# Kernel tuning notes

Measured on AMD Instinct MI355X. Metric: run time of the kernel, lower is better.

Reference implementation:

```python
import jax, jax.numpy as jnp
import numpy as np

B, T, E, H, QKV = 4, 2048, 1024, 16, 64
D = E // H  # head_dim = 64


def setup_inputs() -> dict:
    key = jax.random.key(0)
    k1, k2, k3, k4 = jax.random.split(key, 4)
    scale = 1.0 / np.sqrt(D)
    x = jax.random.normal(k1, (B, T, E), dtype=jnp.float32)
    W_q = jax.random.normal(k2, (QKV, D), dtype=jnp.float32) * scale
    W_k = jax.random.normal(k3, (QKV, D), dtype=jnp.float32) * scale
    W_v = jax.random.normal(k4, (QKV, D), dtype=jnp.float32) * scale
    return {"x": x, "W_q": W_q, "W_k": W_k, "W_v": W_v}


def reference(x, W_q, W_k, W_v):
    Bx, Tx, Ex = x.shape
    d = Ex // H
    # [B,T,E] -> [B,H,T,D]  (same as torch view + permute(0,2,1,3))
    xh = x.reshape(Bx, Tx, H, d).transpose(0, 2, 1, 3)
    # Shared per-head projections: Linear(d -> qkv_dim), weight stored [out,in]
    Q = jnp.einsum("bhtd,qd->bhtq", xh, W_q)
    K = jnp.einsum("bhtd,qd->bhtq", xh, W_k)
    V = jnp.einsum("bhtd,qd->bhtq", xh, W_v)
    # NOTE: original scales by head_dim**0.5, not qkv_dim**0.5
    scores = jnp.einsum("bhtq,bhsq->bhts", Q, K) / jnp.asarray(d, x.dtype) ** 0.5
    attn = jax.nn.softmax(scores, axis=-1)
    out = jnp.einsum("bhts,bhsq->bhtq", attn, V) + V  # attention + V residual
    # per-head concat on last dim == head-major merge: [B,H,T,Q] -> [B,T,H*Q]
    return out.transpose(0, 2, 1, 3).reshape(Bx, Tx, H * W_q.shape[0])
```

## Files before the change

### kernel.cpp

```cpp
#include <hip/hip_runtime.h>

#define T_SEQ 2048
#define N_B   4
#define N_H   16
#define D_H   64
#define EMB   1024
#define CSC   0.18033688011f

typedef __attribute__((ext_vector_type(8))) short   vshort8;
typedef __attribute__((ext_vector_type(4))) float   vfloat4;
typedef __attribute__((ext_vector_type(16))) float  vfloat16;

__device__ __forceinline__ ushort f2bf(float f) {
  union { float f; unsigned u; } v; v.f = f;
  unsigned u = v.u;
  return (ushort)((u + 0x7fffu + ((u >> 16) & 1u)) >> 16);
}
__device__ __forceinline__ unsigned pk2bf(float a, float b) {
  return (unsigned)f2bf(a) | ((unsigned)f2bf(b) << 16);
}
__device__ __forceinline__ float bf2f(ushort b) {
  union { unsigned u; float f; } v; v.u = ((unsigned)b) << 16;
  return v.f;
}
__device__ __forceinline__ float fexp2(float x) {
#if __has_builtin(__builtin_amdgcn_exp2f)
  return __builtin_amdgcn_exp2f(x);
#else
  return exp2f(x);
#endif
}
__device__ __forceinline__ unsigned permhi(float hi, float lo) {
  union { float f; unsigned u; } a, b; a.f = hi; b.f = lo;
#if __has_builtin(__builtin_amdgcn_perm)
  return __builtin_amdgcn_perm(a.u, b.u, 0x07060302u);
#else
  return (a.u & 0xFFFF0000u) | (b.u >> 16);
#endif
}
__device__ __forceinline__ void plswap(unsigned &a, unsigned &b) {
  asm("v_permlane32_swap_b32 %0, %1" : "+v"(a), "+v"(b));
}
__device__ __forceinline__ vshort8 cvt8(const float* p) {
  float4 w0 = *(const float4*)(p);
  float4 w1 = *(const float4*)(p + 4);
  vshort8 t;
  t[0] = (short)f2bf(w0.x); t[1] = (short)f2bf(w0.y);
  t[2] = (short)f2bf(w0.z); t[3] = (short)f2bf(w0.w);
  t[4] = (short)f2bf(w1.x); t[5] = (short)f2bf(w1.y);
  t[6] = (short)f2bf(w1.z); t[7] = (short)f2bf(w1.w);
  return t;
}


__global__ void wconv(const float* __restrict__ Wq, const float* __restrict__ Wk,
                      const float* __restrict__ Wv, ushort* __restrict__ Wb) {
  const int lane = threadIdx.x & 63;
  const int l15  = lane & 15;
  const int quad = lane >> 4;
  const float* Ws[3] = {Wq, Wk, Wv};
#pragma unroll
  for (int m = 0; m < 3; ++m)
#pragma unroll
    for (int kc = 0; kc < 2; ++kc)
#pragma unroll
      for (int nt = 0; nt < 4; ++nt) {
        vshort8 t = cvt8(Ws[m] + (nt * 16 + l15) * D_H + kc * 32 + quad * 8);
        *(vshort8*)(&Wb[(((m * 2 + kc) * 4 + nt) * 64 + lane) * 8]) = t;
      }
}

__global__ __launch_bounds__(256, 4) void proj_qkv(
    const float* __restrict__ x, const ushort* __restrict__ Wb,
    uint2* __restrict__ Qb, uint2* __restrict__ Kb, uint2* __restrict__ Vb) {
  const int wid  = threadIdx.x >> 6;
  const int lane = threadIdx.x & 63;
  const int l15  = lane & 15;
  const int q    = lane >> 4;
  const int gw    = blockIdx.x * 4 + wid;
  const int strip = gw >> 4;
  const int hd    = gw & 15;
  const int r0    = strip * 16;
  const int b     = r0 >> 11;
  const int bh    = b * N_H + hd;
  const int ts    = (r0 & (T_SEQ - 1)) >> 4;

  vshort8 afr[2];
  {
    const float* xp = x + (size_t)(r0 + l15) * EMB + hd * D_H + q * 8;
    afr[0] = cvt8(xp);
    afr[1] = cvt8(xp + 32);
  }

  uint2* Bs[3] = {Qb, Kb, Vb};
#pragma unroll
  for (int m = 0; m < 3; ++m) {
    vshort8 wf[2][4];
#pragma unroll
    for (int kc = 0; kc < 2; ++kc)
#pragma unroll
      for (int nt = 0; nt < 4; ++nt)
        wf[kc][nt] = *(const vshort8*)(&Wb[(((m * 2 + kc) * 4 + nt) * 64 + lane) * 8]);
    vfloat4 acc[4];
#pragma unroll
    for (int nt = 0; nt < 4; ++nt) acc[nt] = (vfloat4){0.f, 0.f, 0.f, 0.f};
#pragma unroll
    for (int kc = 0; kc < 2; ++kc)
#pragma unroll
      for (int nt = 0; nt < 4; ++nt)
        acc[nt] = (m < 2)
          ? __builtin_amdgcn_mfma_f32_16x16x32_bf16(wf[kc][nt], afr[kc], acc[nt], 0, 0, 0)
          : __builtin_amdgcn_mfma_f32_16x16x32_bf16(afr[kc], wf[kc][nt], acc[nt], 0, 0, 0);
    uint2* B = Bs[m];
#pragma unroll
    for (int nt = 0; nt < 4; ++nt) {
      vfloat4 a = acc[nt];
      if (m == 0) { a[0] *= CSC; a[1] *= CSC; a[2] *= CSC; a[3] *= CSC; }
      uint2 w;
      w.x = pk2bf(a[0], a[1]);
      w.y = pk2bf(a[2], a[3]);
      size_t idx;
      if (m < 2) {
        idx = ((size_t)(bh * 64 + (ts >> 1)) * 4 + nt) * 128
              + (l15 + 16 * (ts & 1)) * 4 + q;
      } else {
        idx = (((size_t)(bh * 32 + (ts >> 2)) * 4 + (ts & 3)) * 2 + (nt >> 1)) * 128
              + 64 * (nt & 1) + l15 * 4 + q;
      }
      B[idx] = w;
    }
  }
}

__device__ __forceinline__ void load_k(vshort8 (&kf)[2][4], const uint4* __restrict__ Kb,
                                       int bh, int ss, int lo) {
#pragma unroll
  for (int sb = 0; sb < 2; ++sb)
#pragma unroll
    for (int ds = 0; ds < 4; ++ds)
      kf[sb][ds] = *(const vshort8*)&Kb[((size_t)(bh * 64 + 2 * ss + sb) * 4 + ds) * 64 + lo];
}
__device__ __forceinline__ void load_v(vshort8 (&vf)[4][2], const uint4* __restrict__ Vb,
                                       int bh, int ss, int lo) {
#pragma unroll
  for (int st = 0; st < 4; ++st)
#pragma unroll
    for (int db = 0; db < 2; ++db)
      vf[st][db] = *(const vshort8*)&Vb[(((size_t)(bh * 32 + ss) * 4 + st) * 2 + db) * 64 + lo];
}

__device__ __forceinline__ void tile_compute(
    const vshort8 (&kf)[2][4], const vshort8 (&vf)[4][2], const vshort8 (&qf)[2][4],
    vfloat16 (&oacc)[2][2], float (&lsum)[2], int h) {
#pragma unroll
  for (int tb = 0; tb < 2; ++tb) {
    vfloat16 sacc[2];
#pragma unroll
    for (int sb = 0; sb < 2; ++sb)
#pragma unroll
      for (int i = 0; i < 16; ++i) sacc[sb][i] = 0.f;
#pragma unroll
    for (int sb = 0; sb < 2; ++sb)
#pragma unroll
      for (int ds = 0; ds < 4; ++ds)
        sacc[sb] = __builtin_amdgcn_mfma_f32_32x32x16_bf16(kf[sb][ds], qf[tb][ds], sacc[sb], 0, 0, 0);

    float p[2][16];
    float s0 = 0.f, s1 = 0.f, s2 = 0.f, s3 = 0.f;
#pragma unroll
    for (int sb = 0; sb < 2; ++sb)
#pragma unroll
      for (int r = 0; r < 16; r += 4) {
        p[sb][r + 0] = fexp2(sacc[sb][r + 0]); s0 += p[sb][r + 0];
        p[sb][r + 1] = fexp2(sacc[sb][r + 1]); s1 += p[sb][r + 1];
        p[sb][r + 2] = fexp2(sacc[sb][r + 2]); s2 += p[sb][r + 2];
        p[sb][r + 3] = fexp2(sacc[sb][r + 3]); s3 += p[sb][r + 3];
      }
    lsum[tb] += (s0 + s1) + (s2 + s3);

#pragma unroll
    for (int sb = 0; sb < 2; ++sb)
#pragma unroll
      for (int g = 0; g < 2; ++g) {
        unsigned OL0 = permhi(p[sb][8 * g + 1], p[sb][8 * g + 0]);
        unsigned OL1 = permhi(p[sb][8 * g + 3], p[sb][8 * g + 2]);
        unsigned OH0 = permhi(p[sb][8 * g + 5], p[sb][8 * g + 4]);
        unsigned OH1 = permhi(p[sb][8 * g + 7], p[sb][8 * g + 6]);
        plswap(OL0, OH0);
        plswap(OL1, OH1);
        union { unsigned u[4]; vshort8 v; } pa;
        pa.u[0] = OL0; pa.u[1] = OL1; pa.u[2] = OH0; pa.u[3] = OH1;
        const int st = 2 * sb + g;
#pragma unroll
        for (int db = 0; db < 2; ++db)
          oacc[tb][db] = __builtin_amdgcn_mfma_f32_32x32x16_bf16(pa.v, vf[st][db], oacc[tb][db], 0, 0, 0);
      }
  }
}

__global__ __launch_bounds__(256, 2) void attn_fused(
    const uint4* __restrict__ Qb, const uint4* __restrict__ Kb,
    const uint4* __restrict__ Vb, float* __restrict__ out) {
  const int tid  = threadIdx.x;
  const int wid  = tid >> 6;
  const int lane = tid & 63;
  const int l31  = lane & 31;
  const int h    = lane >> 5;

  const int blk  = blockIdx.x;
  const int work = (blk & 7) * 64 + (blk >> 3);
  const int bh   = work >> 3;
  const int tblk8 = work & 7;
  const int b = bh >> 4, hh = bh & 15;
  const int T64 = tblk8 * 4 + wid;

  const int lo = l31 * 2 + h;

  vshort8 qf[2][4];
#pragma unroll
  for (int tb = 0; tb < 2; ++tb)
#pragma unroll
    for (int ds = 0; ds < 4; ++ds)
      qf[tb][ds] = *(const vshort8*)&Qb[((size_t)(bh * 64 + 2 * T64 + tb) * 4 + ds) * 64 + lo];

  vfloat16 oacc[2][2];
#pragma unroll
  for (int tb = 0; tb < 2; ++tb)
#pragma unroll
    for (int db = 0; db < 2; ++db)
#pragma unroll
      for (int i = 0; i < 16; ++i) oacc[tb][db][i] = 0.f;
  float lsum[2] = {0.f, 0.f};

  vshort8 kfA[2][4], kfB[2][4], vf[4][2];
  load_k(kfA, Kb, bh, 0, lo);

#pragma unroll 1
  for (int ss = 0; ss < 32; ss += 2) {
    load_v(vf, Vb, bh, ss, lo);
    load_k(kfB, Kb, bh, ss + 1, lo);
    tile_compute(kfA, vf, qf, oacc, lsum, h);

    load_v(vf, Vb, bh, ss + 1, lo);
    load_k(kfA, Kb, bh, (ss + 2) & 31, lo);
    tile_compute(kfB, vf, qf, oacc, lsum, h);
  }

  const uint2* Vb2 = (const uint2*)Vb;
#pragma unroll
  for (int tb = 0; tb < 2; ++tb) {
    const float l = lsum[tb] + __shfl_xor(lsum[tb], 32, 64);
    const float inv = 1.0f / l;
    const int T32 = 2 * T64 + tb;
#pragma unroll
    for (int db = 0; db < 2; ++db) {
#pragma unroll
      for (int rq = 0; rq < 4; ++rq) {
        const int sq = 8 * T32 + 2 * rq + h;
        uint2 vr = Vb2[(((size_t)(bh * 32 + (sq >> 4)) * 4 + ((sq >> 2) & 3)) * 2 + db) * 128
                       + l31 * 4 + ((sq >> 1) & 1) * 2 + (sq & 1)];
        float vres[4];
        vres[0] = bf2f((ushort)(vr.x & 0xFFFFu));
        vres[1] = bf2f((ushort)(vr.x >> 16));
        vres[2] = bf2f((ushort)(vr.y & 0xFFFFu));
        vres[3] = bf2f((ushort)(vr.y >> 16));
#pragma unroll
        for (int rr = 0; rr < 4; ++rr) {
          const int row = rr + 8 * rq + 4 * h;
          const float iT = __shfl(inv, row, 64);
          const int t = T32 * 32 + row;
          out[((size_t)(b * T_SEQ + t)) * EMB + hh * D_H + db * 32 + l31] =
              oacc[tb][db][rq * 4 + rr] * iT + vres[rr];
        }
      }
    }
  }
}

extern "C" void kernel_launch(void* const* d_in, const int* in_sizes, int n_in,
                              void* d_out, int out_size, void* d_ws, size_t ws_size,
                              hipStream_t stream) {
  const float* x  = (const float*)d_in[0];
  const float* Wq = (const float*)d_in[1];
  const float* Wk = (const float*)d_in[2];
  const float* Wv = (const float*)d_in[3];
  float* out = (float*)d_out;

  const size_t per4 = (size_t)64 * 64 * 4 * 64;
  uint4* Qb = (uint4*)d_ws;
  uint4* Kb = Qb + per4;
  uint4* Vb = Kb + per4;
  ushort* Wb = (ushort*)(Vb + per4);

  wconv<<<1, 64, 0, stream>>>(Wq, Wk, Wv, Wb);
  proj_qkv<<<2048, 256, 0, stream>>>(x, Wb, (uint2*)Qb, (uint2*)Kb, (uint2*)Vb);
  attn_fused<<<512, 256, 0, stream>>>(Qb, Kb, Vb, out);
}
```

Baseline: 191.8 us.

## Stage K/V tiles through LDS with double-buffered global_load_lds

```diff
diff --git a/kernel.cpp b/kernel.cpp
--- a/kernel.cpp
+++ b/kernel.cpp
@@ -50,6 +50,15 @@
   t[4] = (short)f2bf(w1.x); t[5] = (short)f2bf(w1.y);
   t[6] = (short)f2bf(w1.z); t[7] = (short)f2bf(w1.w);
   return t;
+}
+__device__ __forceinline__ void gload_lds16(const uint4* gp, uint4* lp) {
+  __builtin_amdgcn_global_load_lds(
+      (const __attribute__((address_space(1))) void*)gp,
+      (__attribute__((address_space(3))) void*)lp, 16, 0, 0);
+}
+__device__ __forceinline__ void stage4(const uint4* gp, uint4* lp) {
+#pragma unroll
+  for (int c = 0; c < 4; ++c) gload_lds16(gp + c * 64, lp + c * 64);
 }
 
 
@@ -132,72 +141,6 @@
   }
 }
 
-__device__ __forceinline__ void load_k(vshort8 (&kf)[2][4], const uint4* __restrict__ Kb,
-                                       int bh, int ss, int lo) {
-#pragma unroll
-  for (int sb = 0; sb < 2; ++sb)
-#pragma unroll
-    for (int ds = 0; ds < 4; ++ds)
-      kf[sb][ds] = *(const vshort8*)&Kb[((size_t)(bh * 64 + 2 * ss + sb) * 4 + ds) * 64 + lo];
-}
-__device__ __forceinline__ void load_v(vshort8 (&vf)[4][2], const uint4* __restrict__ Vb,
-                                       int bh, int ss, int lo) {
-#pragma unroll
-  for (int st = 0; st < 4; ++st)
-#pragma unroll
-    for (int db = 0; db < 2; ++db)
-      vf[st][db] = *(const vshort8*)&Vb[(((size_t)(bh * 32 + ss) * 4 + st) * 2 + db) * 64 + lo];
-}
-
-__device__ __forceinline__ void tile_compute(
-    const vshort8 (&kf)[2][4], const vshort8 (&vf)[4][2], const vshort8 (&qf)[2][4],
-    vfloat16 (&oacc)[2][2], float (&lsum)[2], int h) {
-#pragma unroll
-  for (int tb = 0; tb < 2; ++tb) {
-    vfloat16 sacc[2];
-#pragma unroll
-    for (int sb = 0; sb < 2; ++sb)
-#pragma unroll
-      for (int i = 0; i < 16; ++i) sacc[sb][i] = 0.f;
-#pragma unroll
-    for (int sb = 0; sb < 2; ++sb)
-#pragma unroll
-      for (int ds = 0; ds < 4; ++ds)
-        sacc[sb] = __builtin_amdgcn_mfma_f32_32x32x16_bf16(kf[sb][ds], qf[tb][ds], sacc[sb], 0, 0, 0);
-
-    float p[2][16];
-    float s0 = 0.f, s1 = 0.f, s2 = 0.f, s3 = 0.f;
-#pragma unroll
-    for (int sb = 0; sb < 2; ++sb)
-#pragma unroll
-      for (int r = 0; r < 16; r += 4) {
-        p[sb][r + 0] = fexp2(sacc[sb][r + 0]); s0 += p[sb][r + 0];
-        p[sb][r + 1] = fexp2(sacc[sb][r + 1]); s1 += p[sb][r + 1];
-        p[sb][r + 2] = fexp2(sacc[sb][r + 2]); s2 += p[sb][r + 2];
-        p[sb][r + 3] = fexp2(sacc[sb][r + 3]); s3 += p[sb][r + 3];
-      }
-    lsum[tb] += (s0 + s1) + (s2 + s3);
-
-#pragma unroll
-    for (int sb = 0; sb < 2; ++sb)
-#pragma unroll
-      for (int g = 0; g < 2; ++g) {
-        unsigned OL0 = permhi(p[sb][8 * g + 1], p[sb][8 * g + 0]);
-        unsigned OL1 = permhi(p[sb][8 * g + 3], p[sb][8 * g + 2]);
-        unsigned OH0 = permhi(p[sb][8 * g + 5], p[sb][8 * g + 4]);
-        unsigned OH1 = permhi(p[sb][8 * g + 7], p[sb][8 * g + 6]);
-        plswap(OL0, OH0);
-        plswap(OL1, OH1);
-        union { unsigned u[4]; vshort8 v; } pa;
-        pa.u[0] = OL0; pa.u[1] = OL1; pa.u[2] = OH0; pa.u[3] = OH1;
-        const int st = 2 * sb + g;
-#pragma unroll
-        for (int db = 0; db < 2; ++db)
-          oacc[tb][db] = __builtin_amdgcn_mfma_f32_32x32x16_bf16(pa.v, vf[st][db], oacc[tb][db], 0, 0, 0);
-      }
-  }
-}
-
 __global__ __launch_bounds__(256, 2) void attn_fused(
     const uint4* __restrict__ Qb, const uint4* __restrict__ Kb,
     const uint4* __restrict__ Vb, float* __restrict__ out) {
@@ -216,6 +159,16 @@
 
   const int lo = l31 * 2 + h;
 
+  __shared__ uint4 sbuf[2][1024];
+
+  const uint4* gsrc = ((wid < 2) ? Kb : Vb) + (size_t)bh * 16384
+                      + (wid & 1) * 256 + lane;
+  uint4* lds0 = &sbuf[0][wid * 256];
+  uint4* lds1 = &sbuf[1][wid * 256];
+
+  stage4(gsrc, lds0);
+  const uint4* gp = gsrc + 512;
+
   vshort8 qf[2][4];
 #pragma unroll
   for (int tb = 0; tb < 2; ++tb)
@@ -232,18 +185,79 @@
       for (int i = 0; i < 16; ++i) oacc[tb][db][i] = 0.f;
   float lsum[2] = {0.f, 0.f};
 
-  vshort8 kfA[2][4], kfB[2][4], vf[4][2];
-  load_k(kfA, Kb, bh, 0, lo);
+  __syncthreads();
 
 #pragma unroll 1
-  for (int ss = 0; ss < 32; ss += 2) {
-    load_v(vf, Vb, bh, ss, lo);
-    load_k(kfB, Kb, bh, ss + 1, lo);
-    tile_compute(kfA, vf, qf, oacc, lsum, h);
-
-    load_v(vf, Vb, bh, ss + 1, lo);
-    load_k(kfA, Kb, bh, (ss + 2) & 31, lo);
-    tile_compute(kfB, vf, qf, oacc, lsum, h);
+  for (int ss = 0; ss < 32; ++ss) {
+    if (ss < 31) {
+      stage4(gp, (ss & 1) ? lds0 : lds1);
+      gp += 512;
+    }
+    const uint4* lb = sbuf[ss & 1];
+
+    vshort8 kf[2][4];
+#pragma unroll
+    for (int sb = 0; sb < 2; ++sb)
+#pragma unroll
+      for (int ds = 0; ds < 4; ++ds)
+        kf[sb][ds] = *(const vshort8*)&lb[(sb * 4 + ds) * 64 + lo];
+    vshort8 vf[4][2];
+#pragma unroll
+    for (int st = 0; st < 4; ++st)
+#pragma unroll
+      for (int db = 0; db < 2; ++db)
+        vf[st][db] = *(const vshort8*)&lb[512 + (st * 2 + db) * 64 + lo];
+
+#pragma unroll
+    for (int tb = 0; tb < 2; ++tb) {
+      vfloat16 sacc[2];
+#pragma unroll
+      for (int sb = 0; sb < 2; ++sb)
+#pragma unroll
+        for (int i = 0; i < 16; ++i) sacc[sb][i] = 0.f;
+      __builtin_amdgcn_s_setprio(1);
+#pragma unroll
+      for (int sb = 0; sb < 2; ++sb)
+#pragma unroll
+        for (int ds = 0; ds < 4; ++ds)
+          sacc[sb] = __builtin_amdgcn_mfma_f32_32x32x16_bf16(kf[sb][ds], qf[tb][ds], sacc[sb], 0, 0, 0);
+      __builtin_amdgcn_s_setprio(0);
+
+      float p[2][16];
+      float s0 = 0.f, s1 = 0.f, s2 = 0.f, s3 = 0.f;
+#pragma unroll
+      for (int sb = 0; sb < 2; ++sb)
+#pragma unroll
+        for (int r = 0; r < 16; r += 4) {
+          p[sb][r + 0] = fexp2(sacc[sb][r + 0]); s0 += p[sb][r + 0];
+          p[sb][r + 1] = fexp2(sacc[sb][r + 1]); s1 += p[sb][r + 1];
+          p[sb][r + 2] = fexp2(sacc[sb][r + 2]); s2 += p[sb][r + 2];
+          p[sb][r + 3] = fexp2(sacc[sb][r + 3]); s3 += p[sb][r + 3];
+        }
+      lsum[tb] += (s0 + s1) + (s2 + s3);
+
+#pragma unroll
+      for (int sb = 0; sb < 2; ++sb)
+#pragma unroll
+        for (int g = 0; g < 2; ++g) {
+          unsigned OL0 = permhi(p[sb][8 * g + 1], p[sb][8 * g + 0]);
+          unsigned OL1 = permhi(p[sb][8 * g + 3], p[sb][8 * g + 2]);
+          unsigned OH0 = permhi(p[sb][8 * g + 5], p[sb][8 * g + 4]);
+          unsigned OH1 = permhi(p[sb][8 * g + 7], p[sb][8 * g + 6]);
+          plswap(OL0, OH0);
+          plswap(OL1, OH1);
+          union { unsigned u[4]; vshort8 v; } pa;
+          pa.u[0] = OL0; pa.u[1] = OL1; pa.u[2] = OH0; pa.u[3] = OH1;
+          const int st = 2 * sb + g;
+          __builtin_amdgcn_s_setprio(1);
+#pragma unroll
+          for (int db = 0; db < 2; ++db)
+            oacc[tb][db] = __builtin_amdgcn_mfma_f32_32x32x16_bf16(pa.v, vf[st][db], oacc[tb][db], 0, 0, 0);
+          __builtin_amdgcn_s_setprio(0);
+        }
+    }
+
+    __syncthreads();
   }
 
   const uint2* Vb2 = (const uint2*)Vb;
```

New measurement: 175.7 us. -8.4%, faster.
